# Kernel optimization log

Hardware: AMD Instinct MI355X
Metric: run time of the kernel (lower is better)

The kernel has to match this reference:

```python
import jax, jax.numpy as jnp
import numpy as np

DIM = 2048
N_HEADS = 16
N_KV = 4
HEAD_DIM = DIM // N_HEADS  # 128
G = N_HEADS // N_KV        # queries per kv head
EPS = 1e-6
ROPE_BASE = 10000.0


def _rms_norm(x, w):
    # x: [..., head_dim]
    norm = jax.lax.rsqrt(jnp.mean(x * x, axis=-1, keepdims=True) + EPS)
    return x * norm * w


def _rope_tables(seq_len, dtype):
    inv_freq = 1.0 / (ROPE_BASE ** (jnp.arange(0, HEAD_DIM, 2, dtype=jnp.float32) / HEAD_DIM))
    t = jnp.arange(seq_len, dtype=jnp.float32)
    freqs = jnp.einsum('i,j->ij', t, inv_freq)          # [S, hd/2]
    emb = jnp.concatenate([freqs, freqs], axis=-1)       # [S, hd]
    return jnp.cos(emb).astype(dtype), jnp.sin(emb).astype(dtype)


def _rotate_half(x):
    x1, x2 = x[..., : HEAD_DIM // 2], x[..., HEAD_DIM // 2:]
    return jnp.concatenate([-x2, x1], axis=-1)


def setup_inputs() -> dict:
    key = jax.random.key(0)
    ks = jax.random.split(key, 7)
    x = jax.random.normal(ks[0], (2, 2048, DIM), dtype=jnp.float32)
    s = 0.02
    Wq = jax.random.normal(ks[1], (DIM, DIM), dtype=jnp.float32) * s
    Wk = jax.random.normal(ks[2], (DIM, N_KV * HEAD_DIM), dtype=jnp.float32) * s
    Wv = jax.random.normal(ks[3], (DIM, N_KV * HEAD_DIM), dtype=jnp.float32) * s
    Wo = jax.random.normal(ks[4], (DIM, DIM), dtype=jnp.float32) * s
    q_norm_w = jnp.ones((HEAD_DIM,), dtype=jnp.float32)
    k_norm_w = jnp.ones((HEAD_DIM,), dtype=jnp.float32)
    return {"x": x, "Wq": Wq, "Wk": Wk, "Wv": Wv, "Wo": Wo,
            "q_norm_w": q_norm_w, "k_norm_w": k_norm_w}


def reference(x, Wq, Wk, Wv, Wo, q_norm_w, k_norm_w):
    B, S, _ = x.shape
    q = (x @ Wq).reshape(B, S, N_HEADS, HEAD_DIM)
    k = (x @ Wk).reshape(B, S, N_KV, HEAD_DIM)
    v = (x @ Wv).reshape(B, S, N_KV, HEAD_DIM)

    q = _rms_norm(q, q_norm_w)
    k = _rms_norm(k, k_norm_w)

    q = q.transpose(0, 2, 1, 3)  # [B, H, S, hd]
    k = k.transpose(0, 2, 1, 3)  # [B, KV, S, hd]
    v = v.transpose(0, 2, 1, 3)

    cos, sin = _rope_tables(S, x.dtype)  # [S, hd], broadcasts over B,H
    q = q * cos + _rotate_half(q) * sin
    k = k * cos + _rotate_half(k) * sin

    # GQA: group queries by kv head instead of repeating K/V (same math as repeat_interleave)
    qg = q.reshape(B, N_KV, G, S, HEAD_DIM)
    scale = HEAD_DIM ** -0.5
    scores = jnp.einsum('bkgqd,bkkd2->bkgqk2'.replace('k2', 'K').replace('d2', 'd'),
                        qg, k) if False else jnp.einsum('bkgqd,bkKd->bkgqK', qg, k) * scale
    attn = jax.nn.softmax(scores, axis=-1)               # [B, KV, G, S, S]
    out = jnp.einsum('bkgqK,bkKd->bkgqd', attn, v)       # [B, KV, G, S, hd]
    out = out.reshape(B, N_HEADS, S, HEAD_DIM).transpose(0, 2, 1, 3).reshape(B, S, DIM)
    return out @ Wo
```

## Files before the change

### kernel.cpp

```cpp
#include <hip/hip_runtime.h>
#include <stdint.h>

#define LOG2E 1.4426950408889634f

typedef __attribute__((ext_vector_type(8))) short short8;
typedef __attribute__((ext_vector_type(4))) float floatx4;
typedef unsigned int u32;

__device__ __forceinline__ float bf2f(unsigned short h) {
  union { unsigned int u; float f; } v; v.u = ((unsigned int)h) << 16; return v.f;
}
__device__ __forceinline__ unsigned short f2bf(float f) {
  union { float f; unsigned int u; } v; v.f = f;
  unsigned int r = v.u + 0x7FFFu + ((v.u >> 16) & 1u);
  return (unsigned short)(r >> 16);
}
__device__ __forceinline__ u32 fbits(float f) {
  union { float f; u32 u; } v; v.f = f; return v.u;
}
__device__ __forceinline__ void async16(void* lds, const void* g) {
  __builtin_amdgcn_global_load_lds((const __attribute__((address_space(1))) u32*)g,
                                   (__attribute__((address_space(3))) u32*)lds, 16, 0, 0);
}

__global__ __launch_bounds__(256) void prep(const float* __restrict__ x,
                                            const float* __restrict__ Wq,
                                            const float* __restrict__ Wk,
                                            const float* __restrict__ Wv,
                                            const float* __restrict__ Wo,
                                            unsigned short* __restrict__ xbf,
                                            unsigned short* __restrict__ WTqkv,
                                            unsigned short* __restrict__ WoT) {
  __shared__ unsigned short tile[64][65];
  int bid = blockIdx.x;
  if (bid < 4096) {
    int i = (bid * 256 + threadIdx.x) * 8;
    float4 a = ((const float4*)(x + i))[0];
    float4 b = ((const float4*)(x + i))[1];
    union { uint4 v; unsigned short u[8]; } o;
    o.u[0] = f2bf(a.x); o.u[1] = f2bf(a.y); o.u[2] = f2bf(a.z); o.u[3] = f2bf(a.w);
    o.u[4] = f2bf(b.x); o.u[5] = f2bf(b.y); o.u[6] = f2bf(b.z); o.u[7] = f2bf(b.w);
    *(uint4*)(xbf + i) = o.v;
    return;
  }
  bid -= 4096;
  const int R = 2048;
  const float* src; unsigned short* dst; int C;
  if (bid < 1024) { src = Wq; dst = WTqkv; C = 2048; }
  else if (bid < 1280) { src = Wk; dst = WTqkv + (size_t)2048 * 2048; C = 512; bid -= 1024; }
  else if (bid < 1536) { src = Wv; dst = WTqkv + (size_t)2048 * 2048 + (size_t)512 * 2048; C = 512; bid -= 1280; }
  else { src = Wo; dst = WoT; C = 2048; bid -= 1536; }
  int tc = C >> 6;
  int br = bid / tc, bc = bid % tc;
  int r0 = br << 6, c0 = bc << 6;
  int i = threadIdx.x >> 2, cc = (threadIdx.x & 3) << 4;
  const float4* g = (const float4*)(src + (size_t)(r0 + i) * C + c0 + cc);
  float4 f0 = g[0], f1 = g[1], f2 = g[2], f3 = g[3];
  unsigned short u[16];
  u[0]=f2bf(f0.x); u[1]=f2bf(f0.y); u[2]=f2bf(f0.z); u[3]=f2bf(f0.w);
  u[4]=f2bf(f1.x); u[5]=f2bf(f1.y); u[6]=f2bf(f1.z); u[7]=f2bf(f1.w);
  u[8]=f2bf(f2.x); u[9]=f2bf(f2.y); u[10]=f2bf(f2.z); u[11]=f2bf(f2.w);
  u[12]=f2bf(f3.x); u[13]=f2bf(f3.y); u[14]=f2bf(f3.z); u[15]=f2bf(f3.w);
#pragma unroll
  for (int j = 0; j < 16; ++j) tile[i][cc + j] = u[j];
  __syncthreads();
  union { uint4 v[2]; unsigned short u[16]; } buf;
#pragma unroll
  for (int j = 0; j < 16; ++j) buf.u[j] = tile[cc + j][i];
  uint4* o = (uint4*)(dst + (size_t)(c0 + i) * R + r0 + cc);
  o[0] = buf.v[0]; o[1] = buf.v[1];
}

template <typename OutT>
__global__ __launch_bounds__(256) void gemm_nt(const unsigned short* __restrict__ A,
                                               const unsigned short* __restrict__ BT,
                                               OutT* __restrict__ C,
                                               int M, int N, int K) {
  __shared__ unsigned short As[2][128 * 32];
  __shared__ unsigned short Bs[2][128 * 32];
  const int nb = N >> 7;
  const int bnn = nb >> 3;
  const int xcd = blockIdx.x & 7;
  const int idx = blockIdx.x >> 3;
  const int bn = (idx % bnn) * 8 + xcd;
  const int bm = idx / bnn;
  const int m0 = bm << 7, n0 = bn << 7;
  const int tid = threadIdx.x;
  const int lane = tid & 63, wave = tid >> 6;
  const int l15 = lane & 15, quad = lane >> 4;
  const int wm = (wave >> 1) << 6, wn = (wave & 1) << 6;

  floatx4 acc[4][4];
#pragma unroll
  for (int i = 0; i < 4; ++i)
#pragma unroll
    for (int j = 0; j < 4; ++j) acc[i][j] = (floatx4){0.f, 0.f, 0.f, 0.f};

  const int Lc0 = wave * 128 + lane;
#pragma unroll
  for (int i = 0; i < 2; ++i) {
    int Lc = Lc0 + i * 64;
    int row = Lc >> 2;
    int c = (lane & 3) ^ ((row >> 1) & 3);
    async16(As[0] + (size_t)Lc * 8, A + (size_t)(m0 + row) * K + c * 8);
    async16(Bs[0] + (size_t)Lc * 8, BT + (size_t)(n0 + row) * K + c * 8);
  }

  const int nk = K >> 5;
  for (int it = 0; it < nk; ++it) {
    const int cur = it & 1;
    __syncthreads();
    if (it + 1 < nk) {
      int k1 = (it + 1) << 5;
#pragma unroll
      for (int i = 0; i < 2; ++i) {
        int Lc = Lc0 + i * 64;
        int row = Lc >> 2;
        int c = (lane & 3) ^ ((row >> 1) & 3);
        async16(As[cur ^ 1] + (size_t)Lc * 8, A + (size_t)(m0 + row) * K + k1 + c * 8);
        async16(Bs[cur ^ 1] + (size_t)Lc * 8, BT + (size_t)(n0 + row) * K + k1 + c * 8);
      }
    }
    short8 af[4], bf[4];
#pragma unroll
    for (int mt = 0; mt < 4; ++mt) {
      int m = wm + mt * 16 + l15;
      af[mt] = *(const short8*)(&As[cur][(m * 4 + (quad ^ ((m >> 1) & 3))) * 8]);
    }
#pragma unroll
    for (int nt = 0; nt < 4; ++nt) {
      int n = wn + nt * 16 + l15;
      bf[nt] = *(const short8*)(&Bs[cur][(n * 4 + (quad ^ ((n >> 1) & 3))) * 8]);
    }
#pragma unroll
    for (int mt = 0; mt < 4; ++mt)
#pragma unroll
      for (int nt = 0; nt < 4; ++nt)
        acc[mt][nt] = __builtin_amdgcn_mfma_f32_16x16x32_bf16(af[mt], bf[nt], acc[mt][nt], 0, 0, 0);
  }
#pragma unroll
  for (int mt = 0; mt < 4; ++mt)
#pragma unroll
    for (int nt = 0; nt < 4; ++nt)
#pragma unroll
      for (int r = 0; r < 4; ++r) {
        int m = m0 + wm + mt * 16 + quad * 4 + r;
        int n = n0 + wn + nt * 16 + l15;
        float v = acc[mt][nt][r];
        if constexpr (sizeof(OutT) == 2)
          C[(size_t)m * N + n] = (OutT)f2bf(v);
        else
          C[(size_t)m * N + n] = (OutT)v;
      }
}

__global__ __launch_bounds__(256) void post_qkv(const unsigned short* __restrict__ qkv,
                                                const float* __restrict__ qw,
                                                const float* __restrict__ kw,
                                                unsigned short* __restrict__ qT,
                                                unsigned short* __restrict__ kT,
                                                unsigned short* __restrict__ vT) {
  const int S = 2048;
  __shared__ unsigned short tile[64][65];
  int bid = blockIdx.x;
  if (bid < 20480) {
    int wid = bid * 4 + (threadIdx.x >> 6);
    int lane = threadIdx.x & 63;
    int slot = wid % 20;
    int bs = wid / 20;
    int s = bs & (S - 1), b = bs >> 11;
    const unsigned short* src;
    unsigned short* dst;
    const float* w;
    float scale;
    if (slot < 16) {
      src = qkv + (size_t)bs * 3072 + slot * 128;
      dst = qT + ((size_t)(b * 16 + slot) * S + s) * 128;
      w = qw; scale = 0.08838834764831845f * 1.4426950408889634f;
    } else {
      int kvi = slot - 16;
      src = qkv + (size_t)bs * 3072 + 2048 + kvi * 128;
      dst = kT + ((size_t)(b * 4 + kvi) * S + s) * 128;
      w = kw; scale = 1.0f;
    }
    float x1 = bf2f(src[lane]), x2 = bf2f(src[lane + 64]);
    float ss = x1 * x1 + x2 * x2;
#pragma unroll
    for (int m = 1; m < 64; m <<= 1) ss += __shfl_xor(ss, m, 64);
    float rms = rsqrtf(ss * (1.0f / 128.0f) + 1e-6f);
    float y1 = x1 * rms * w[lane];
    float y2 = x2 * rms * w[lane + 64];
    float ang = (float)s * exp2f((float)lane * -0.2076205059304601f);
    float c = cosf(ang), sn = sinf(ang);
    float o1 = (y1 * c - y2 * sn) * scale;
    float o2 = (y2 * c + y1 * sn) * scale;
    dst[lane] = f2bf(o1);
    dst[lane + 64] = f2bf(o2);
    return;
  }
  bid -= 20480;
  int dt = bid & 1, st = (bid >> 1) & 31, kv = (bid >> 6) & 3, b = bid >> 8;
  int s0 = st << 6, d0 = dt << 6;
  int i = threadIdx.x >> 2, cc = (threadIdx.x & 3) << 4;
  union { uint4 v[2]; unsigned short u[16]; } buf;
  const uint4* g = (const uint4*)(qkv + ((size_t)(b * S) + s0 + i) * 3072 + 2560 + kv * 128 + d0 + cc);
  buf.v[0] = g[0]; buf.v[1] = g[1];
#pragma unroll
  for (int j = 0; j < 16; ++j) tile[i][cc + j] = buf.u[j];
  __syncthreads();
#pragma unroll
  for (int j = 0; j < 16; ++j) buf.u[j] = tile[cc + j][i];
  uint4* o = (uint4*)(vT + ((size_t)(b * 4 + kv) * 128 + d0 + i) * S + s0 + cc);
  o[0] = buf.v[0]; o[1] = buf.v[1];
}

__global__ __launch_bounds__(256, 2) void flash_attn(const unsigned short* __restrict__ qT,
                                                     const unsigned short* __restrict__ kT,
                                                     const unsigned short* __restrict__ vT,
                                                     unsigned short* __restrict__ ao) {
  const int S = 2048;
  int bid = blockIdx.x;
  int grp = bid & 7, inner = bid >> 3;
  int b = grp >> 2, kv = grp & 3;
  int h = kv * 4 + (inner & 3);
  int qt = inner >> 2;
  int tid = threadIdx.x;
  int lane = tid & 63, wave = tid >> 6;
  int l15 = lane & 15, quad = lane >> 4;

  __shared__ unsigned short Ks[2][64 * 128];
  __shared__ unsigned short VTs[2][128 * 64];
  __shared__ unsigned short Ps[4][32 * 64];
  unsigned short* Psw = Ps[wave];

  short8 bq[2][4];
  const unsigned short* qbase = qT + ((size_t)(b * 16 + h) * S + qt * 128 + wave * 32) * 128;
#pragma unroll
  for (int nt = 0; nt < 2; ++nt)
#pragma unroll
    for (int kk = 0; kk < 4; ++kk)
      bq[nt][kk] = *(const short8*)(qbase + (size_t)(nt * 16 + l15) * 128 + kk * 32 + quad * 8);

  floatx4 O[2][8];
#pragma unroll
  for (int mt = 0; mt < 2; ++mt)
#pragma unroll
    for (int dt = 0; dt < 8; ++dt) O[mt][dt] = (floatx4){0.f, 0.f, 0.f, 0.f};
  float l_acc[2] = {0.f, 0.f};

  const size_t kbase = (size_t)(b * 4 + kv) * S * 128;
  const size_t vbase = (size_t)(b * 4 + kv) * 128 * S;

#pragma unroll
  for (int i = 0; i < 4; ++i) {
    int Lc = (wave * 4 + i) * 64 + lane;
    int row = Lc >> 4, cjk = (lane & 15) ^ (row & 7);
    async16(Ks[0] + (size_t)Lc * 8, kT + kbase + (size_t)row * 128 + cjk * 8);
    int d = Lc >> 3, cjv = (lane & 7) ^ (d & 7);
    async16(VTs[0] + (size_t)Lc * 8, vT + vbase + (size_t)d * S + cjv * 8);
  }

  for (int kt = 0; kt < 32; ++kt) {
    int cur = kt & 1;
    __syncthreads();
    if (kt + 1 < 32) {
#pragma unroll
      for (int i = 0; i < 4; ++i) {
        int Lc = (wave * 4 + i) * 64 + lane;
        int row = Lc >> 4, cjk = (lane & 15) ^ (row & 7);
        async16(Ks[cur ^ 1] + (size_t)Lc * 8,
                kT + kbase + (size_t)((kt + 1) * 64 + row) * 128 + cjk * 8);
        int d = Lc >> 3, cjv = (lane & 7) ^ (d & 7);
        async16(VTs[cur ^ 1] + (size_t)Lc * 8,
                vT + vbase + (size_t)d * S + (kt + 1) * 64 + cjv * 8);
      }
    }

    floatx4 st[4][2];
#pragma unroll
    for (int a = 0; a < 4; ++a)
#pragma unroll
      for (int nt = 0; nt < 2; ++nt) st[a][nt] = (floatx4){0.f, 0.f, 0.f, 0.f};
#pragma unroll
    for (int kk = 0; kk < 4; ++kk)
#pragma unroll
      for (int a = 0; a < 4; ++a) {
        int m = a * 16 + l15;
        short8 ak = *(const short8*)(&Ks[cur][(m * 16 + ((kk * 4 + quad) ^ (m & 7))) * 8]);
#pragma unroll
        for (int nt = 0; nt < 2; ++nt)
          st[a][nt] = __builtin_amdgcn_mfma_f32_16x16x32_bf16(ak, bq[nt][kk], st[a][nt], 0, 0, 0);
      }

#pragma unroll
    for (int nt = 0; nt < 2; ++nt) {
      int m = nt * 16 + l15;
#pragma unroll
      for (int a = 0; a < 4; ++a) {
        float e0 = __builtin_amdgcn_exp2f(st[a][nt][0]);
        float e1 = __builtin_amdgcn_exp2f(st[a][nt][1]);
        float e2 = __builtin_amdgcn_exp2f(st[a][nt][2]);
        float e3 = __builtin_amdgcn_exp2f(st[a][nt][3]);
        l_acc[nt] += (e0 + e1) + (e2 + e3);
        u32 p01 = __builtin_amdgcn_perm(fbits(e1) + 0x8000u, fbits(e0) + 0x8000u, 0x07060302u);
        u32 p23 = __builtin_amdgcn_perm(fbits(e3) + 0x8000u, fbits(e2) + 0x8000u, 0x07060302u);
        int c = (a * 2 + (quad >> 1)) ^ (m & 7);
        uint2 pk; pk.x = p01; pk.y = p23;
        *(uint2*)(&Psw[(m * 8 + c) * 8 + (quad & 1) * 4]) = pk;
      }
    }

#pragma unroll
    for (int kk2 = 0; kk2 < 2; ++kk2) {
      short8 ap[2];
#pragma unroll
      for (int mt = 0; mt < 2; ++mt) {
        int m = mt * 16 + l15;
        ap[mt] = *(const short8*)(&Psw[(m * 8 + ((kk2 * 4 + quad) ^ (m & 7))) * 8]);
      }
#pragma unroll
      for (int dt = 0; dt < 8; ++dt) {
        int n = dt * 16 + l15;
        short8 bv = *(const short8*)(&VTs[cur][(n * 8 + ((kk2 * 4 + quad) ^ (n & 7))) * 8]);
#pragma unroll
        for (int mt = 0; mt < 2; ++mt)
          O[mt][dt] = __builtin_amdgcn_mfma_f32_16x16x32_bf16(ap[mt], bv, O[mt][dt], 0, 0, 0);
      }
    }
  }

  float linv[2];
#pragma unroll
  for (int nt = 0; nt < 2; ++nt) {
    float l = l_acc[nt];
    l += __shfl_xor(l, 16, 64);
    l += __shfl_xor(l, 32, 64);
    linv[nt] = 1.f / l;
  }
#pragma unroll
  for (int mt = 0; mt < 2; ++mt)
#pragma unroll
    for (int r = 0; r < 4; ++r) {
      float inv = __shfl(linv[mt], quad * 4 + r, 64);
      int s = qt * 128 + wave * 32 + mt * 16 + quad * 4 + r;
#pragma unroll
      for (int dt = 0; dt < 8; ++dt) {
        int d = dt * 16 + l15;
        ao[((size_t)(b * S + s) * 16 + h) * 128 + d] = f2bf(O[mt][dt][r] * inv);
      }
    }
}

extern "C" void kernel_launch(void* const* d_in, const int* in_sizes, int n_in,
                              void* d_out, int out_size, void* d_ws, size_t ws_size,
                              hipStream_t stream) {
  const float* x  = (const float*)d_in[0];
  const float* Wq = (const float*)d_in[1];
  const float* Wk = (const float*)d_in[2];
  const float* Wv = (const float*)d_in[3];
  const float* Wo = (const float*)d_in[4];
  const float* qw = (const float*)d_in[5];
  const float* kw = (const float*)d_in[6];
  float* out = (float*)d_out;

  unsigned short* p = (unsigned short*)d_ws;
  unsigned short* xbf   = p; p += (size_t)4096 * 2048;
  unsigned short* WTqkv = p; p += (size_t)3072 * 2048;
  unsigned short* WoT   = p; p += (size_t)2048 * 2048;
  unsigned short* qkv   = p; p += (size_t)4096 * 3072;
  unsigned short* qTb   = p; p += (size_t)2 * 16 * 2048 * 128;
  unsigned short* kTb   = p; p += (size_t)2 * 4 * 2048 * 128;
  unsigned short* vTb   = p; p += (size_t)2 * 4 * 2048 * 128;
  unsigned short* ao    = p; p += (size_t)4096 * 2048;

  prep<<<6656, 256, 0, stream>>>(x, Wq, Wk, Wv, Wo, xbf, WTqkv, WoT);

  gemm_nt<unsigned short><<<768, 256, 0, stream>>>(xbf, WTqkv, qkv, 4096, 3072, 2048);

  post_qkv<<<20992, 256, 0, stream>>>(qkv, qw, kw, qTb, kTb, vTb);

  flash_attn<<<512, 256, 0, stream>>>(qTb, kTb, vTb, ao);

  gemm_nt<float><<<512, 256, 0, stream>>>(ao, WoT, out, 4096, 2048, 2048);
}
```

Measured before the change: 330.1 us.

## Fuse RMSNorm, RoPE and V transpose into QKV GEMM; enlarge attention query tile

A new gemm_qkv kernel gives each block a full 128-wide head column. It applies RMSNorm, RoPE and scaling in the epilogue for Q and K, and transposes V through LDS, which removes the bf16 qkv intermediate and the separate post_qkv pass. Flash attention now handles 256 queries per block (64 per wave) with launch bounds of one block, halving the grid to 256 blocks. This reuses each K/V tile across more queries but raises register pressure and lowers occupancy.

```diff
diff --git a/kernel.cpp b/kernel.cpp
--- a/kernel.cpp
+++ b/kernel.cpp
@@ -1,7 +1,5 @@
 #include <hip/hip_runtime.h>
 #include <stdint.h>
-
-#define LOG2E 1.4426950408889634f
 
 typedef __attribute__((ext_vector_type(8))) short short8;
 typedef __attribute__((ext_vector_type(4))) float floatx4;
@@ -71,10 +69,149 @@
   o[0] = buf.v[0]; o[1] = buf.v[1];
 }
 
-template <typename OutT>
+__global__ __launch_bounds__(256) void gemm_qkv(const unsigned short* __restrict__ A,
+                                                const unsigned short* __restrict__ BT,
+                                                const float* __restrict__ qw,
+                                                const float* __restrict__ kw,
+                                                unsigned short* __restrict__ qT,
+                                                unsigned short* __restrict__ kT,
+                                                unsigned short* __restrict__ vT) {
+  const int K = 2048;
+  __shared__ unsigned short smem[16384];
+  unsigned short* As = smem;
+  unsigned short* Bs = smem + 8192;
+  const int xcd = blockIdx.x & 7;
+  const int idx = blockIdx.x >> 3;
+  const int bn = (idx % 3) * 8 + xcd;
+  const int bm = idx / 3;
+  const int m0 = bm << 7, n0 = bn << 7;
+  const int tid = threadIdx.x;
+  const int lane = tid & 63, wave = tid >> 6;
+  const int l15 = lane & 15, quad = lane >> 4;
+  const int wr = wave << 5;
+
+  float w8[8];
+  if (bn < 20) {
+    const float* wsrc = (bn < 16) ? qw : kw;
+#pragma unroll
+    for (int nt = 0; nt < 8; ++nt) w8[nt] = wsrc[nt * 16 + l15];
+  }
+  float invf[4];
+#pragma unroll
+  for (int j = 0; j < 4; ++j)
+    invf[j] = exp2f((float)(j * 16 + l15) * -0.2076205059304601f);
+
+  floatx4 acc[2][8];
+#pragma unroll
+  for (int i = 0; i < 2; ++i)
+#pragma unroll
+    for (int j = 0; j < 8; ++j) acc[i][j] = (floatx4){0.f, 0.f, 0.f, 0.f};
+
+  const int Lc0 = wave * 128 + lane;
+#pragma unroll
+  for (int i = 0; i < 2; ++i) {
+    int Lc = Lc0 + i * 64;
+    int row = Lc >> 2;
+    int c = (lane & 3) ^ ((row >> 1) & 3);
+    async16(As + (size_t)Lc * 8, A + (size_t)(m0 + row) * K + c * 8);
+    async16(Bs + (size_t)Lc * 8, BT + (size_t)(n0 + row) * K + c * 8);
+  }
+  for (int it = 0; it < 64; ++it) {
+    const int cur = it & 1;
+    __syncthreads();
+    if (it + 1 < 64) {
+      int k1 = (it + 1) << 5;
+#pragma unroll
+      for (int i = 0; i < 2; ++i) {
+        int Lc = Lc0 + i * 64;
+        int row = Lc >> 2;
+        int c = (lane & 3) ^ ((row >> 1) & 3);
+        async16(As + (cur ^ 1) * 4096 + (size_t)Lc * 8, A + (size_t)(m0 + row) * K + k1 + c * 8);
+        async16(Bs + (cur ^ 1) * 4096 + (size_t)Lc * 8, BT + (size_t)(n0 + row) * K + k1 + c * 8);
+      }
+    }
+    short8 af[2], bf[8];
+#pragma unroll
+    for (int mt = 0; mt < 2; ++mt) {
+      int m = wr + mt * 16 + l15;
+      af[mt] = *(const short8*)(&As[cur * 4096 + (m * 4 + (quad ^ ((m >> 1) & 3))) * 8]);
+    }
+#pragma unroll
+    for (int nt = 0; nt < 8; ++nt) {
+      int n = nt * 16 + l15;
+      bf[nt] = *(const short8*)(&Bs[cur * 4096 + (n * 4 + (quad ^ ((n >> 1) & 3))) * 8]);
+    }
+#pragma unroll
+    for (int mt = 0; mt < 2; ++mt)
+#pragma unroll
+      for (int nt = 0; nt < 8; ++nt)
+        acc[mt][nt] = __builtin_amdgcn_mfma_f32_16x16x32_bf16(af[mt], bf[nt], acc[mt][nt], 0, 0, 0);
+  }
+
+  if (bn < 20) {
+    const bool isq = bn < 16;
+    const float sc = isq ? (0.08838834764831845f * 1.4426950408889634f) : 1.0f;
+    unsigned short* dbase = isq ? (qT + (size_t)bn * 2048 * 128)
+                                : (kT + (size_t)(bn - 16) * 2048 * 128);
+#pragma unroll
+    for (int mt = 0; mt < 2; ++mt)
+#pragma unroll
+      for (int r = 0; r < 4; ++r) {
+        float ssq = 0.f;
+#pragma unroll
+        for (int nt = 0; nt < 8; ++nt) ssq += acc[mt][nt][r] * acc[mt][nt][r];
+#pragma unroll
+        for (int m = 1; m < 16; m <<= 1) ssq += __shfl_xor(ssq, m, 64);
+        float rms = rsqrtf(ssq * (1.0f / 128.0f) + 1e-6f);
+        int s_glob = m0 + wr + mt * 16 + quad * 4 + r;
+        int b = s_glob >> 11, s = s_glob & 2047;
+        float y[8];
+#pragma unroll
+        for (int nt = 0; nt < 8; ++nt) y[nt] = acc[mt][nt][r] * rms * w8[nt];
+        unsigned short* drow = dbase + ((size_t)b * (isq ? 16 : 4) * 2048 + s) * 128;
+#pragma unroll
+        for (int j = 0; j < 4; ++j) {
+          float ang = (float)s * invf[j];
+          float c = cosf(ang), sn = sinf(ang);
+          float lo = (y[j] * c - y[j + 4] * sn) * sc;
+          float hi = (y[j + 4] * c + y[j] * sn) * sc;
+          drow[j * 16 + l15] = f2bf(lo);
+          drow[(j + 4) * 16 + l15] = f2bf(hi);
+        }
+      }
+  } else {
+    const int kv = bn - 20;
+    const int b = m0 >> 11, s0 = m0 & 2047;
+    __syncthreads();
+    unsigned short* T = smem;
+#pragma unroll
+    for (int mt = 0; mt < 2; ++mt)
+#pragma unroll
+      for (int nt = 0; nt < 8; ++nt) {
+        int d = nt * 16 + l15;
+        int ch = wave * 4 + mt * 2 + (quad >> 1);
+        int cs = ch ^ (d & 15);
+        u32 p01 = __builtin_amdgcn_perm(fbits(acc[mt][nt][1]) + 0x8000u,
+                                        fbits(acc[mt][nt][0]) + 0x8000u, 0x07060302u);
+        u32 p23 = __builtin_amdgcn_perm(fbits(acc[mt][nt][3]) + 0x8000u,
+                                        fbits(acc[mt][nt][2]) + 0x8000u, 0x07060302u);
+        uint2 pk; pk.x = p01; pk.y = p23;
+        *(uint2*)(&T[d * 128 + cs * 8 + (quad & 1) * 4]) = pk;
+      }
+    __syncthreads();
+#pragma unroll
+    for (int j = 0; j < 8; ++j) {
+      int d = tid >> 1, cpos = (tid & 1) * 8 + j;
+      int cs = cpos ^ (d & 15);
+      uint4 val = *(const uint4*)(&T[d * 128 + cs * 8]);
+      *(uint4*)(vT + ((size_t)(b * 4 + kv) * 128 + d) * 2048 + s0 + cpos * 8) = val;
+    }
+  }
+}
+
 __global__ __launch_bounds__(256) void gemm_nt(const unsigned short* __restrict__ A,
                                                const unsigned short* __restrict__ BT,
-                                               OutT* __restrict__ C,
+                                               float* __restrict__ C,
                                                int M, int N, int K) {
   __shared__ unsigned short As[2][128 * 32];
   __shared__ unsigned short Bs[2][128 * 32];
@@ -105,7 +242,6 @@
     async16(As[0] + (size_t)Lc * 8, A + (size_t)(m0 + row) * K + c * 8);
     async16(Bs[0] + (size_t)Lc * 8, BT + (size_t)(n0 + row) * K + c * 8);
   }
-
   const int nk = K >> 5;
   for (int it = 0; it < nk; ++it) {
     const int cur = it & 1;
@@ -146,75 +282,11 @@
       for (int r = 0; r < 4; ++r) {
         int m = m0 + wm + mt * 16 + quad * 4 + r;
         int n = n0 + wn + nt * 16 + l15;
-        float v = acc[mt][nt][r];
-        if constexpr (sizeof(OutT) == 2)
-          C[(size_t)m * N + n] = (OutT)f2bf(v);
-        else
-          C[(size_t)m * N + n] = (OutT)v;
-      }
-}
-
-__global__ __launch_bounds__(256) void post_qkv(const unsigned short* __restrict__ qkv,
-                                                const float* __restrict__ qw,
-                                                const float* __restrict__ kw,
-                                                unsigned short* __restrict__ qT,
-                                                unsigned short* __restrict__ kT,
-                                                unsigned short* __restrict__ vT) {
-  const int S = 2048;
-  __shared__ unsigned short tile[64][65];
-  int bid = blockIdx.x;
-  if (bid < 20480) {
-    int wid = bid * 4 + (threadIdx.x >> 6);
-    int lane = threadIdx.x & 63;
-    int slot = wid % 20;
-    int bs = wid / 20;
-    int s = bs & (S - 1), b = bs >> 11;
-    const unsigned short* src;
-    unsigned short* dst;
-    const float* w;
-    float scale;
-    if (slot < 16) {
-      src = qkv + (size_t)bs * 3072 + slot * 128;
-      dst = qT + ((size_t)(b * 16 + slot) * S + s) * 128;
-      w = qw; scale = 0.08838834764831845f * 1.4426950408889634f;
-    } else {
-      int kvi = slot - 16;
-      src = qkv + (size_t)bs * 3072 + 2048 + kvi * 128;
-      dst = kT + ((size_t)(b * 4 + kvi) * S + s) * 128;
-      w = kw; scale = 1.0f;
-    }
-    float x1 = bf2f(src[lane]), x2 = bf2f(src[lane + 64]);
-    float ss = x1 * x1 + x2 * x2;
-#pragma unroll
-    for (int m = 1; m < 64; m <<= 1) ss += __shfl_xor(ss, m, 64);
-    float rms = rsqrtf(ss * (1.0f / 128.0f) + 1e-6f);
-    float y1 = x1 * rms * w[lane];
-    float y2 = x2 * rms * w[lane + 64];
-    float ang = (float)s * exp2f((float)lane * -0.2076205059304601f);
-    float c = cosf(ang), sn = sinf(ang);
-    float o1 = (y1 * c - y2 * sn) * scale;
-    float o2 = (y2 * c + y1 * sn) * scale;
-    dst[lane] = f2bf(o1);
-    dst[lane + 64] = f2bf(o2);
-    return;
-  }
-  bid -= 20480;
-  int dt = bid & 1, st = (bid >> 1) & 31, kv = (bid >> 6) & 3, b = bid >> 8;
-  int s0 = st << 6, d0 = dt << 6;
-  int i = threadIdx.x >> 2, cc = (threadIdx.x & 3) << 4;
-  union { uint4 v[2]; unsigned short u[16]; } buf;
-  const uint4* g = (const uint4*)(qkv + ((size_t)(b * S) + s0 + i) * 3072 + 2560 + kv * 128 + d0 + cc);
-  buf.v[0] = g[0]; buf.v[1] = g[1];
-#pragma unroll
-  for (int j = 0; j < 16; ++j) tile[i][cc + j] = buf.u[j];
-  __syncthreads();
-#pragma unroll
-  for (int j = 0; j < 16; ++j) buf.u[j] = tile[cc + j][i];
-  uint4* o = (uint4*)(vT + ((size_t)(b * 4 + kv) * 128 + d0 + i) * S + s0 + cc);
-  o[0] = buf.v[0]; o[1] = buf.v[1];
-}
-
-__global__ __launch_bounds__(256, 2) void flash_attn(const unsigned short* __restrict__ qT,
+        C[(size_t)m * N + n] = acc[mt][nt][r];
+      }
+}
+
+__global__ __launch_bounds__(256, 1) void flash_attn(const unsigned short* __restrict__ qT,
                                                      const unsigned short* __restrict__ kT,
                                                      const unsigned short* __restrict__ vT,
                                                      unsigned short* __restrict__ ao) {
@@ -230,23 +302,23 @@
 
   __shared__ unsigned short Ks[2][64 * 128];
   __shared__ unsigned short VTs[2][128 * 64];
-  __shared__ unsigned short Ps[4][32 * 64];
+  __shared__ unsigned short Ps[4][64 * 64];
   unsigned short* Psw = Ps[wave];
 
-  short8 bq[2][4];
-  const unsigned short* qbase = qT + ((size_t)(b * 16 + h) * S + qt * 128 + wave * 32) * 128;
-#pragma unroll
-  for (int nt = 0; nt < 2; ++nt)
+  short8 bq[4][4];
+  const unsigned short* qbase = qT + ((size_t)(b * 16 + h) * S + qt * 256 + wave * 64) * 128;
+#pragma unroll
+  for (int nt = 0; nt < 4; ++nt)
 #pragma unroll
     for (int kk = 0; kk < 4; ++kk)
       bq[nt][kk] = *(const short8*)(qbase + (size_t)(nt * 16 + l15) * 128 + kk * 32 + quad * 8);
 
-  floatx4 O[2][8];
-#pragma unroll
-  for (int mt = 0; mt < 2; ++mt)
+  floatx4 O[4][8];
+#pragma unroll
+  for (int mt = 0; mt < 4; ++mt)
 #pragma unroll
     for (int dt = 0; dt < 8; ++dt) O[mt][dt] = (floatx4){0.f, 0.f, 0.f, 0.f};
-  float l_acc[2] = {0.f, 0.f};
+  float l_acc[4] = {0.f, 0.f, 0.f, 0.f};
 
   const size_t kbase = (size_t)(b * 4 + kv) * S * 128;
   const size_t vbase = (size_t)(b * 4 + kv) * 128 * S;
@@ -276,11 +348,11 @@
       }
     }
 
-    floatx4 st[4][2];
+    floatx4 st[4][4];
 #pragma unroll
     for (int a = 0; a < 4; ++a)
 #pragma unroll
-      for (int nt = 0; nt < 2; ++nt) st[a][nt] = (floatx4){0.f, 0.f, 0.f, 0.f};
+      for (int nt = 0; nt < 4; ++nt) st[a][nt] = (floatx4){0.f, 0.f, 0.f, 0.f};
 #pragma unroll
     for (int kk = 0; kk < 4; ++kk)
 #pragma unroll
@@ -288,12 +360,12 @@
         int m = a * 16 + l15;
         short8 ak = *(const short8*)(&Ks[cur][(m * 16 + ((kk * 4 + quad) ^ (m & 7))) * 8]);
 #pragma unroll
-        for (int nt = 0; nt < 2; ++nt)
+        for (int nt = 0; nt < 4; ++nt)
           st[a][nt] = __builtin_amdgcn_mfma_f32_16x16x32_bf16(ak, bq[nt][kk], st[a][nt], 0, 0, 0);
       }
 
 #pragma unroll
-    for (int nt = 0; nt < 2; ++nt) {
+    for (int nt = 0; nt < 4; ++nt) {
       int m = nt * 16 + l15;
 #pragma unroll
       for (int a = 0; a < 4; ++a) {
@@ -312,9 +384,9 @@
 
 #pragma unroll
     for (int kk2 = 0; kk2 < 2; ++kk2) {
-      short8 ap[2];
-#pragma unroll
-      for (int mt = 0; mt < 2; ++mt) {
+      short8 ap[4];
+#pragma unroll
+      for (int mt = 0; mt < 4; ++mt) {
         int m = mt * 16 + l15;
         ap[mt] = *(const short8*)(&Psw[(m * 8 + ((kk2 * 4 + quad) ^ (m & 7))) * 8]);
       }
@@ -323,26 +395,26 @@
         int n = dt * 16 + l15;
         short8 bv = *(const short8*)(&VTs[cur][(n * 8 + ((kk2 * 4 + quad) ^ (n & 7))) * 8]);
 #pragma unroll
-        for (int mt = 0; mt < 2; ++mt)
+        for (int mt = 0; mt < 4; ++mt)
           O[mt][dt] = __builtin_amdgcn_mfma_f32_16x16x32_bf16(ap[mt], bv, O[mt][dt], 0, 0, 0);
       }
     }
   }
 
-  float linv[2];
-#pragma unroll
-  for (int nt = 0; nt < 2; ++nt) {
+  float linv[4];
+#pragma unroll
+  for (int nt = 0; nt < 4; ++nt) {
     float l = l_acc[nt];
     l += __shfl_xor(l, 16, 64);
     l += __shfl_xor(l, 32, 64);
     linv[nt] = 1.f / l;
   }
 #pragma unroll
-  for (int mt = 0; mt < 2; ++mt)
+  for (int mt = 0; mt < 4; ++mt)
 #pragma unroll
     for (int r = 0; r < 4; ++r) {
       float inv = __shfl(linv[mt], quad * 4 + r, 64);
-      int s = qt * 128 + wave * 32 + mt * 16 + quad * 4 + r;
+      int s = qt * 256 + wave * 64 + mt * 16 + quad * 4 + r;
 #pragma unroll
       for (int dt = 0; dt < 8; ++dt) {
         int d = dt * 16 + l15;
@@ -367,7 +439,6 @@
   unsigned short* xbf   = p; p += (size_t)4096 * 2048;
   unsigned short* WTqkv = p; p += (size_t)3072 * 2048;
   unsigned short* WoT   = p; p += (size_t)2048 * 2048;
-  unsigned short* qkv   = p; p += (size_t)4096 * 3072;
   unsigned short* qTb   = p; p += (size_t)2 * 16 * 2048 * 128;
   unsigned short* kTb   = p; p += (size_t)2 * 4 * 2048 * 128;
   unsigned short* vTb   = p; p += (size_t)2 * 4 * 2048 * 128;
@@ -375,11 +446,9 @@
 
   prep<<<6656, 256, 0, stream>>>(x, Wq, Wk, Wv, Wo, xbf, WTqkv, WoT);
 
-  gemm_nt<unsigned short><<<768, 256, 0, stream>>>(xbf, WTqkv, qkv, 4096, 3072, 2048);
-
-  post_qkv<<<20992, 256, 0, stream>>>(qkv, qw, kw, qTb, kTb, vTb);
-
-  flash_attn<<<512, 256, 0, stream>>>(qTb, kTb, vTb, ao);
-
-  gemm_nt<float><<<512, 256, 0, stream>>>(ao, WoT, out, 4096, 2048, 2048);
-}
+  gemm_qkv<<<768, 256, 0, stream>>>(xbf, WTqkv, qw, kw, qTb, kTb, vTb);
+
+  flash_attn<<<256, 256, 0, stream>>>(qTb, kTb, vTb, ao);
+
+  gemm_nt<<<512, 256, 0, stream>>>(ao, WoT, out, 4096, 2048, 2048);
+}
```

Result: slower. 731.5 us (+121.6%).
